# Performance work log

Hardware: AMD Instinct MI355X
Metric: run time of the kernel (lower is better)

## Reference

```python
import jax, jax.numpy as jnp
import numpy as np

B, N, HID, EPOCH = 16, 512, 32, 201


def setup_inputs() -> dict:
    key = jax.random.key(0)
    k1, k2, k3, k4 = jax.random.split(key, 4)
    f = jax.random.normal(k1, (B, 1, N, N), dtype=jnp.float32)
    # per-sample 3x3 stencil: perturbed 5-point Laplacian, positive center for stable Jacobi
    base = jnp.array([[0., -1., 0.], [-1., 4., -1.], [0., -1., 0.]], dtype=jnp.float32)
    kernelA = base[None, None] + 0.1 * jax.random.normal(k2, (B, 1, 3, 3), dtype=jnp.float32)
    kernelA = kernelA.at[:, :, 1, 1].set(jnp.maximum(kernelA[:, :, 1, 1], 1.0))
    u = jnp.zeros((B, 1, N, N), jnp.float32)
    # stand-in DeepONet H: pointwise 2 -> HID -> 1 MLP on concat(LFA, residual)
    W1 = 0.1 * jax.random.normal(k3, (HID, 2), dtype=jnp.float32)
    b1 = jnp.zeros((HID,), jnp.float32)
    W2 = 0.1 * jax.random.normal(k4, (1, HID), dtype=jnp.float32)
    b2 = jnp.zeros((1,), jnp.float32)
    return {"f": f, "kernelA": kernelA, "u": u, "W1": W1, "b1": b1, "W2": W2, "b2": b2, "epoch": EPOCH}


def _A(x, kernel):
    # per-sample 3x3 stencil: batch dim mapped to channels, grouped conv (groups = B)
    bsz = x.shape[0]
    y = jax.lax.conv_general_dilated(
        jnp.transpose(x, (1, 0, 2, 3)), kernel, (1, 1), ((1, 1), (1, 1)),
        dimension_numbers=("NCHW", "OIHW", "NCHW"), feature_group_count=bsz)
    return jnp.transpose(y, (1, 0, 2, 3))


def _lfa(kernelA, n):
    # ComputeSmootherFactor: Jacobi symbol |prod_j (1 - tau * A_hat(theta))| on the frequency grid
    h = 1.0 / (n + 1)
    p = np.arange(-(n // 2), n // 2)
    P1, P2 = np.meshgrid(p, p)
    t1 = jnp.asarray(2j * np.pi * h * P1, jnp.complex64)
    t2 = jnp.asarray(2j * np.pi * h * P2, jnp.complex64)
    E = jnp.stack([
        jnp.exp(-t1 - t2), jnp.exp(-t2), jnp.exp(t1 - t2),
        jnp.exp(-t1), jnp.ones_like(t1), jnp.exp(t1),
        jnp.exp(-t1 + t2), jnp.exp(t2), jnp.exp(t1 + t2)])  # [9,N,N]
    bsz = kernelA.shape[0]
    S = jnp.einsum("bk,kxy->bxy", kernelA.reshape(bsz, 9).astype(jnp.complex64), E)
    tau = (0.5 / kernelA[:, 0, 1, 1]).astype(jnp.complex64)[:, None, None]
    y = (1.0 - tau * S) ** 5  # 5 identical Jacobi factors
    return jnp.abs(y)[:, None].astype(jnp.float32)  # [B,1,N,N]


def _H(lfa, r, W1, b1, W2, b2):
    # pointwise MLP correction operator (stand-in for DeepONet)
    z = jnp.concatenate([lfa, r], axis=1)  # [B,2,N,N]
    hdn = jax.nn.gelu(jnp.einsum("bcxy,oc->boxy", z, W1) + b1[None, :, None, None])
    return jnp.einsum("bcxy,oc->boxy", hdn, W2) + b2[None, :, None, None]


def reference(f, kernelA, u, W1, b1, W2, b2, epoch):
    K = (epoch - 1) // 100 + 1
    n = f.shape[-1]
    lfa = _lfa(kernelA, n)
    taus = 0.5 / kernelA[:, :, 1:2, 1:2]  # [B,1,1,1], w=0.5
    x = jnp.zeros_like(f)
    for _ in range(K):
        for _ in range(10):  # jacobi, M=10
            x = x + taus * (f - _A(x, kernelA))
        r = f - _A(x, kernelA)
        x = x + _H(lfa, r, W1, b1, W2, b2)
    r = f - _A(x, kernelA)
    return jnp.linalg.norm(r) / jnp.linalg.norm(f)
```

## Files before the change

### kernel.cpp

```cpp
#include <hip/hip_runtime.h>
#include <math.h>

#define BB 16
#define NN 512
#define HID 32

#define HALO 16
#define TW 96
#define TWP 97
#define OT 64

#define GELU_K1 (-2.302208201f)
#define GELU_K2 (-0.102944244f)

#define CDR 0.99992499f
#define SDR 0.012247618f
#define REVS 0.0019493177f

__global__ __launch_bounds__(256) void lfa_kernel(const float* __restrict__ kernelA,
                                                  float* __restrict__ lfa) {
    const int t = threadIdx.x;
    const int strip = t & 127;
    const int i = blockIdx.y * 2 + (t >> 7);
    const int b = blockIdx.z;
    const int j0 = strip * 4;
    const float* a = kernelA + b * 9;
    float a0 = a[0], a1 = a[1], a2 = a[2], a3 = a[3], a4 = a[4];
    float a5 = a[5], a6 = a[6], a7 = a[7], a8 = a[8];
    const float A35 = a3 + a5, A17 = a1 + a7, A08 = a0 + a8, A26 = a2 + a6;
    const float B53 = a5 - a3, B71 = a7 - a1, B80 = a8 - a0, B26 = a2 - a6;
    const float tau = 0.5f / a4;

    float r1 = (float)(j0 - NN / 2) * REVS;
    float r2 = (float)(i - NN / 2) * REVS;
    float s1 = __builtin_amdgcn_sinf(r1);
    float c1 = __builtin_amdgcn_cosf(r1);
    float s2 = __builtin_amdgcn_sinf(r2);
    float c2 = __builtin_amdgcn_cosf(r2);

    float out[4];
#pragma unroll
    for (int k = 0; k < 4; ++k) {
        float cc = c1 * c2, ss = s1 * s2, sc = s1 * c2, cs = c1 * s2;
        float cpp = cc - ss, cpm = cc + ss, spp = sc + cs, spm = sc - cs;
        float re = fmaf(A35, c1, a4); re = fmaf(A17, c2, re);
        re = fmaf(A08, cpp, re);      re = fmaf(A26, cpm, re);
        float im = B53 * s1;          im = fmaf(B71, s2, im);
        im = fmaf(B80, spp, im);      im = fmaf(B26, spm, im);
        float zre = fmaf(-tau, re, 1.0f);
        float zim = tau * im;
        float m2 = fmaf(zre, zre, zim * zim);
        out[k] = m2 * m2 * sqrtf(m2);
        float tt = s1 * SDR;
        float ns = fmaf(s1, CDR, c1 * SDR);
        c1 = fmaf(c1, CDR, -tt);
        s1 = ns;
    }
    float4 ov = {out[0], out[1], out[2], out[3]};
    *(float4*)(lfa + (size_t)b * NN * NN + (size_t)i * NN + j0) = ov;
}

template <bool FIRST, bool RES>
__global__ __launch_bounds__(256) void fused_cycle(
        const float* __restrict__ xin, float* __restrict__ xout,
        const float* __restrict__ f, const float* __restrict__ kernelA,
        const float* __restrict__ lfa,
        const float* __restrict__ W1, const float* __restrict__ b1,
        const float* __restrict__ W2, const float* __restrict__ b2,
        float* __restrict__ accp, float* __restrict__ outp) {
    __shared__ float sxraw[98 * TWP + 2];
    float* sx = sxraw + TWP + 1;
    const int tx = threadIdx.x;
    const int ty = threadIdx.y;
    const int t  = ty * 32 + tx;
    const int b  = blockIdx.z;
    const int gy0 = blockIdx.y * OT;
    const int gx0 = blockIdx.x * OT;
    const int goi = gy0 - HALO;
    const int goj = gx0 - HALO;
    const float* fg = f + (size_t)b * NN * NN;
    const float* ag = kernelA + b * 9;
    const float ar0 = ag[0], ar1 = ag[1], ar2 = ag[2], ar3 = ag[3], ar4 = ag[4];
    const float ar5 = ag[5], ar6 = ag[6], ar7 = ag[7], ar8 = ag[8];
    const float tau = 0.5f / ar4;
    const float s0 = tau * ar0, q1 = tau * ar1, q2 = tau * ar2, q3 = tau * ar3;
    const float q4 = tau * ar4, q5 = tau * ar5, q6 = tau * ar6, q7 = tau * ar7;
    const float q8 = tau * ar8;

    if (FIRST) {
        if (t == 0 && (blockIdx.x | blockIdx.y | blockIdx.z) == 0) {
            accp[0] = 0.f;
            accp[1] = 0.f;
            ((unsigned int*)accp)[2] = 0u;
        }
    }

    if (t < 98) sxraw[t] = 0.f;
    if (t < 96) sxraw[97 + 97 * t] = 0.f;
    if (t < 98) sxraw[9409 + t] = 0.f;

    if (!FIRST) {
        const float* xg = xin + (size_t)b * NN * NN;
#pragma unroll
        for (int k = 0; k < 9; ++k) {
            int idx = t + k * 256;
            int row = idx / 24;
            int c4  = (idx - row * 24) * 4;
            int gi = goi + row, gj = goj + c4;
            float4 v = {0.f, 0.f, 0.f, 0.f};
            if ((unsigned)gi < NN && (unsigned)gj < NN)
                v = *(const float4*)(xg + (size_t)gi * NN + gj);
            float* d = sx + row * TWP + c4;
            d[0] = v.x; d[1] = v.y; d[2] = v.z; d[3] = v.w;
        }
    }

    const int R0 = ty * 12, C0 = tx * 3;

    const float* pb  = sx + (R0 - 1) * TWP + (C0 - 1);
    float*       pwv = sx + R0 * TWP + C0;

    float vR[12], vC[3];
#pragma unroll
    for (int r = 0; r < 12; ++r) {
        int R = R0 + r, gi = goi + R;
        vR[r] = (R >= 1 && R < TW - 1 && gi >= 0 && gi < NN) ? 1.f : 0.f;
    }
#pragma unroll
    for (int c = 0; c < 3; ++c) {
        int C = C0 + c, gj = goj + C;
        vC[c] = (C >= 1 && C < TW - 1 && gj >= 0 && gj < NN) ? 1.f : 0.f;
    }

    float frt[12][3];
#pragma unroll
    for (int r = 0; r < 12; ++r) {
        int gi = goi + R0 + r;
#pragma unroll
        for (int c = 0; c < 3; ++c) {
            int gj = goj + C0 + c;
            frt[r][c] = (gi >= 0 && gi < NN && gj >= 0 && gj < NN)
                            ? tau * fg[gi * NN + gj] : 0.f;
        }
    }

    __syncthreads();

    float cur[12][3];
    if (FIRST) {
#pragma unroll
        for (int r = 0; r < 12; ++r) {
#pragma unroll
            for (int c = 0; c < 3; ++c)
                cur[r][c] = (vR[r] * vC[c]) * frt[r][c];
        }
        pwv[0] = cur[0][0]; pwv[1] = cur[0][1]; pwv[2] = cur[0][2];
        pwv[11 * TWP] = cur[11][0]; pwv[11 * TWP + 1] = cur[11][1];
        pwv[11 * TWP + 2] = cur[11][2];
#pragma unroll
        for (int r = 1; r < 11; ++r) {
            pwv[r * TWP] = cur[r][0];
            pwv[r * TWP + 2] = cur[r][2];
        }
        __syncthreads();
    } else {
#pragma unroll
        for (int r = 0; r < 12; ++r) {
            cur[r][0] = pwv[r * TWP];
            cur[r][1] = pwv[r * TWP + 1];
            cur[r][2] = pwv[r * TWP + 2];
        }
    }

    for (int s = FIRST ? 1 : 0; s < 10; ++s) {
        float top0 = pb[0], top1 = pb[1], top2 = pb[2], top3 = pb[3], top4 = pb[4];
        float bot0 = pb[13 * TWP],     bot1 = pb[13 * TWP + 1],
              bot2 = pb[13 * TWP + 2], bot3 = pb[13 * TWP + 3],
              bot4 = pb[13 * TWP + 4];
        float pm0 = top1, pm1v = top2, pm2 = top3;
        float Lm1 = top0, Rm1 = top4;
        float Lc = pb[TWP], Rc = pb[TWP + 4];
#pragma unroll
        for (int r = 0; r < 12; ++r) {
            float n0, n1, n2, Lp, Rp;
            if (r < 11) {
                n0 = cur[r + 1][0]; n1 = cur[r + 1][1]; n2 = cur[r + 1][2];
                Lp = pb[(r + 2) * TWP];
                Rp = pb[(r + 2) * TWP + 4];
            } else {
                n0 = bot1; n1 = bot2; n2 = bot3; Lp = bot0; Rp = bot4;
            }
            float o0 = cur[r][0], o1 = cur[r][1], o2 = cur[r][2];
            {
                float ax = s0 * Lm1;
                ax = fmaf(q1, pm0, ax); ax = fmaf(q2, pm1v, ax);
                ax = fmaf(q3, Lc, ax);  ax = fmaf(q4, o0, ax);
                ax = fmaf(q5, o1, ax);  ax = fmaf(q6, Lp, ax);
                ax = fmaf(q7, n0, ax);  ax = fmaf(q8, n1, ax);
                cur[r][0] = fmaf(vR[r] * vC[0], frt[r][0] - ax, o0);
            }
            {
                float ax = s0 * pm0;
                ax = fmaf(q1, pm1v, ax); ax = fmaf(q2, pm2, ax);
                ax = fmaf(q3, o0, ax);   ax = fmaf(q4, o1, ax);
                ax = fmaf(q5, o2, ax);   ax = fmaf(q6, n0, ax);
                ax = fmaf(q7, n1, ax);   ax = fmaf(q8, n2, ax);
                cur[r][1] = fmaf(vR[r] * vC[1], frt[r][1] - ax, o1);
            }
            {
                float ax = s0 * pm1v;
                ax = fmaf(q1, pm2, ax); ax = fmaf(q2, Rm1, ax);
                ax = fmaf(q3, o1, ax);  ax = fmaf(q4, o2, ax);
                ax = fmaf(q5, Rc, ax);  ax = fmaf(q6, n1, ax);
                ax = fmaf(q8, Rp, fmaf(q7, n2, ax));
                cur[r][2] = fmaf(vR[r] * vC[2], frt[r][2] - ax, o2);
            }
            pm0 = o0; pm1v = o1; pm2 = o2;
            Lm1 = Lc; Rm1 = Rc; Lc = Lp; Rc = Rp;
        }
        __syncthreads();
        if (s < 9) {
            pwv[0] = cur[0][0]; pwv[1] = cur[0][1]; pwv[2] = cur[0][2];
            pwv[11 * TWP] = cur[11][0]; pwv[11 * TWP + 1] = cur[11][1];
            pwv[11 * TWP + 2] = cur[11][2];
#pragma unroll
            for (int r = 1; r < 11; ++r) {
                pwv[r * TWP] = cur[r][0];
                pwv[r * TWP + 2] = cur[r][2];
            }
        } else {
#pragma unroll
            for (int r = 0; r < 12; ++r) {
                pwv[r * TWP] = cur[r][0];
                pwv[r * TWP + 1] = cur[r][1];
                pwv[r * TWP + 2] = cur[r][2];
            }
        }
        __syncthreads();
    }

    const int orow = t >> 2;
    const int oseg = t & 3;
    const int Rl = HALO + orow;
    const int Cl0 = HALO + oseg * 16;
    const float* pw = sx + (Rl - 1) * TWP + (Cl0 - 1);
    const int gi = gy0 + orow;
    const int gjb = gx0 + oseg * 16;
    const float b2v = b2[0];

    if (!RES) {
        float w0[18], w1[18], w2[18];
#pragma unroll
        for (int k = 0; k < 18; ++k) {
            w0[k] = pw[k];
            w1[k] = pw[TWP + k];
            w2[k] = pw[2 * TWP + k];
        }
        const float4* f4 = (const float4*)(fg + (size_t)gi * NN + gjb);
        const float4* l4 = (const float4*)(lfa + (size_t)b * NN * NN + (size_t)gi * NN + gjb);
        float fv[16], lv[16];
#pragma unroll
        for (int q = 0; q < 4; ++q) {
            float4 fq = f4[q], lq = l4[q];
            fv[q * 4] = fq.x; fv[q * 4 + 1] = fq.y; fv[q * 4 + 2] = fq.z; fv[q * 4 + 3] = fq.w;
            lv[q * 4] = lq.x; lv[q * 4 + 1] = lq.y; lv[q * 4 + 2] = lq.z; lv[q * 4 + 3] = lq.w;
        }
        float rv[16];
#pragma unroll
        for (int k = 0; k < 16; ++k) {
            float ax = ar0 * w0[k];
            ax = fmaf(ar1, w0[k + 1], ax); ax = fmaf(ar2, w0[k + 2], ax);
            ax = fmaf(ar3, w1[k], ax);     ax = fmaf(ar4, w1[k + 1], ax);
            ax = fmaf(ar5, w1[k + 2], ax); ax = fmaf(ar6, w2[k], ax);
            ax = fmaf(ar7, w2[k + 1], ax); ax = fmaf(ar8, w2[k + 2], ax);
            rv[k] = fv[k] - ax;
        }
        float acc[16];
#pragma unroll
        for (int k = 0; k < 16; ++k) acc[k] = 0.f;
        for (int hh = 0; hh < HID; ++hh) {
            float w1a = W1[2 * hh], w1b = W1[2 * hh + 1], bb = b1[hh], wo = W2[hh];
#pragma unroll
            for (int k = 0; k < 16; ++k) {
                float v = fmaf(w1a, lv[k], fmaf(w1b, rv[k], bb));
                float m = v * fmaf(GELU_K2, v * v, GELU_K1);
                float e = __builtin_amdgcn_exp2f(m);
                float g = v * __builtin_amdgcn_rcpf(1.0f + e);
                acc[k] = fmaf(wo, g, acc[k]);
            }
        }
        float4* xo4 = (float4*)(xout + (size_t)b * NN * NN + (size_t)gi * NN + gjb);
#pragma unroll
        for (int q = 0; q < 4; ++q) {
            float4 ov;
            ov.x = w1[q * 4 + 1] + acc[q * 4] + b2v;
            ov.y = w1[q * 4 + 2] + acc[q * 4 + 1] + b2v;
            ov.z = w1[q * 4 + 3] + acc[q * 4 + 2] + b2v;
            ov.w = w1[q * 4 + 4] + acc[q * 4 + 3] + b2v;
            xo4[q] = ov;
        }
    } else {
        float rv[16];
        {
            float w[18];
#pragma unroll
            for (int k = 0; k < 18; ++k) w[k] = pw[k];
#pragma unroll
            for (int k = 0; k < 16; ++k) {
                float ax = ar0 * w[k];
                ax = fmaf(ar1, w[k + 1], ax);
                rv[k] = fmaf(ar2, w[k + 2], ax);
            }
#pragma unroll
            for (int k = 0; k < 18; ++k) w[k] = pw[TWP + k];
#pragma unroll
            for (int k = 0; k < 16; ++k) {
                float ax = fmaf(ar3, w[k], rv[k]);
                ax = fmaf(ar4, w[k + 1], ax);
                rv[k] = fmaf(ar5, w[k + 2], ax);
            }
#pragma unroll
            for (int k = 0; k < 18; ++k) w[k] = pw[2 * TWP + k];
#pragma unroll
            for (int k = 0; k < 16; ++k) {
                float ax = fmaf(ar6, w[k], rv[k]);
                ax = fmaf(ar7, w[k + 1], ax);
                rv[k] = fmaf(ar8, w[k + 2], ax);
            }
        }
        float f2 = 0.f;
        {
            const float4* f4 = (const float4*)(fg + (size_t)gi * NN + gjb);
#pragma unroll
            for (int q = 0; q < 4; ++q) {
                float4 fq = f4[q];
                rv[q * 4]     = fq.x - rv[q * 4];
                rv[q * 4 + 1] = fq.y - rv[q * 4 + 1];
                rv[q * 4 + 2] = fq.z - rv[q * 4 + 2];
                rv[q * 4 + 3] = fq.w - rv[q * 4 + 3];
                f2 = fmaf(fq.x, fq.x, f2);
                f2 = fmaf(fq.y, fq.y, f2);
                f2 = fmaf(fq.z, fq.z, f2);
                f2 = fmaf(fq.w, fq.w, f2);
            }
        }

        float Hr0 = 0.f, Hr1 = 0.f;
        int hoff0 = 0, hoff1 = 0;
        auto ringH = [&](int rc, float& Hv, int& hoff) {
            int R, C;
            if (rc < 66)       { R = 15; C = 15 + rc; }
            else if (rc < 132) { R = 80; C = rc - 51; }
            else if (rc < 196) { R = rc - 116; C = 15; }
            else               { R = rc - 180; C = 80; }
            hoff = R * TWP + C;
            int rgi = goi + R, rgj = goj + C;
            Hv = 0.f;
            if (rgi >= 0 && rgi < NN && rgj >= 0 && rgj < NN) {
                const float* pr = sx + (R - 1) * TWP + (C - 1);
                float u0 = pr[0], u1 = pr[1], u2 = pr[2];
                float m0 = pr[TWP], m1 = pr[TWP + 1], m2 = pr[TWP + 2];
                float d0 = pr[2 * TWP], d1 = pr[2 * TWP + 1], d2 = pr[2 * TWP + 2];
                float ax = ar0 * u0;
                ax = fmaf(ar1, u1, ax); ax = fmaf(ar2, u2, ax);
                ax = fmaf(ar3, m0, ax); ax = fmaf(ar4, m1, ax);
                ax = fmaf(ar5, m2, ax); ax = fmaf(ar6, d0, ax);
                ax = fmaf(ar7, d1, ax); ax = fmaf(ar8, d2, ax);
                float rp = fg[(size_t)rgi * NN + rgj] - ax;
                float lf = lfa[(size_t)b * NN * NN + (size_t)rgi * NN + rgj];
                float av = 0.f;
                for (int hh = 0; hh < HID; ++hh) {
                    float w1a = W1[2 * hh], w1b = W1[2 * hh + 1], bbv = b1[hh], wo = W2[hh];
                    float v = fmaf(w1a, lf, fmaf(w1b, rp, bbv));
                    float m = v * fmaf(GELU_K2, v * v, GELU_K1);
                    float e = __builtin_amdgcn_exp2f(m);
                    float gg = v * __builtin_amdgcn_rcpf(1.0f + e);
                    av = fmaf(wo, gg, av);
                }
                Hv = av + b2v;
            }
        };
        ringH(t, Hr0, hoff0);
        if (t < 4) ringH(t + 256, Hr1, hoff1);

        float acc[16];
#pragma unroll
        for (int k = 0; k < 16; ++k) acc[k] = 0.f;
        {
            float lv[16];
            const float4* l4 = (const float4*)(lfa + (size_t)b * NN * NN + (size_t)gi * NN + gjb);
#pragma unroll
            for (int q = 0; q < 4; ++q) {
                float4 lq = l4[q];
                lv[q * 4] = lq.x; lv[q * 4 + 1] = lq.y;
                lv[q * 4 + 2] = lq.z; lv[q * 4 + 3] = lq.w;
            }
            for (int hh = 0; hh < HID; ++hh) {
                float w1a = W1[2 * hh], w1b = W1[2 * hh + 1], bb = b1[hh], wo = W2[hh];
#pragma unroll
                for (int k = 0; k < 16; ++k) {
                    float v = fmaf(w1a, lv[k], fmaf(w1b, rv[k], bb));
                    float m = v * fmaf(GELU_K2, v * v, GELU_K1);
                    float e = __builtin_amdgcn_exp2f(m);
                    float g = v * __builtin_amdgcn_rcpf(1.0f + e);
                    acc[k] = fmaf(wo, g, acc[k]);
                }
            }
        }

        __syncthreads();
        float* ph = sx + Rl * TWP + Cl0;
#pragma unroll
        for (int k = 0; k < 16; ++k) ph[k] = acc[k] + b2v;
        sx[hoff0] = Hr0;
        if (t < 4) sx[hoff1] = Hr1;
        __syncthreads();

        float rr = 0.f;
        {
            float hr[18];
#pragma unroll
            for (int k = 0; k < 18; ++k) hr[k] = pw[k];
#pragma unroll
            for (int k = 0; k < 16; ++k) {
                float ax = ar0 * hr[k];
                ax = fmaf(ar1, hr[k + 1], ax);
                ax = fmaf(ar2, hr[k + 2], ax);
                rv[k] -= ax;
            }
#pragma unroll
            for (int k = 0; k < 18; ++k) hr[k] = pw[TWP + k];
#pragma unroll
            for (int k = 0; k < 16; ++k) {
                float ax = ar3 * hr[k];
                ax = fmaf(ar4, hr[k + 1], ax);
                ax = fmaf(ar5, hr[k + 2], ax);
                rv[k] -= ax;
            }
#pragma unroll
            for (int k = 0; k < 18; ++k) hr[k] = pw[2 * TWP + k];
#pragma unroll
            for (int k = 0; k < 16; ++k) {
                float ax = ar6 * hr[k];
                ax = fmaf(ar7, hr[k + 1], ax);
                ax = fmaf(ar8, hr[k + 2], ax);
                float r = rv[k] - ax;
                rr = fmaf(r, r, rr);
            }
        }
#pragma unroll
        for (int off = 32; off > 0; off >>= 1) {
            rr += __shfl_down(rr, off, 64);
            f2 += __shfl_down(f2, off, 64);
        }
        if ((t & 63) == 0) { sxraw[t >> 6] = rr; sxraw[4 + (t >> 6)] = f2; }
        __syncthreads();
        if (t == 0) {
            atomicAdd(&accp[0], sxraw[0] + sxraw[1] + sxraw[2] + sxraw[3]);
            atomicAdd(&accp[1], sxraw[4] + sxraw[5] + sxraw[6] + sxraw[7]);
            __threadfence();
            unsigned int done = atomicAdd((unsigned int*)accp + 2, 1u);
            if (done == (NN / OT) * (NN / OT) * BB - 1) {
                __threadfence();
                float rrt = atomicAdd(&accp[0], 0.f);
                float fft = atomicAdd(&accp[1], 0.f);
                outp[0] = sqrtf(rrt / fft);
            }
        }
    }
}

extern "C" void kernel_launch(void* const* d_in, const int* in_sizes, int n_in,
                              void* d_out, int out_size, void* d_ws, size_t ws_size,
                              hipStream_t stream) {
    const float* f  = (const float*)d_in[0];
    const float* kA = (const float*)d_in[1];
    float*       u  = (float*)d_in[2];
    const float* W1 = (const float*)d_in[3];
    const float* b1 = (const float*)d_in[4];
    const float* W2 = (const float*)d_in[5];
    const float* b2 = (const float*)d_in[6];
    float* out = (float*)d_out;

    char* ws = (char*)d_ws;
    float* acc = (float*)ws;
    float* xB  = (float*)(ws + 256);
    float* lfa = (float*)(ws + 256 + (size_t)BB * NN * NN * 4);

    lfa_kernel<<<dim3(1, NN / 2, BB), 256, 0, stream>>>(kA, lfa);

    dim3 jblk(32, 8);
    dim3 jgrd(NN / OT, NN / OT, BB);

    fused_cycle<true,  false><<<jgrd, jblk, 0, stream>>>(u, xB, f, kA, lfa, W1, b1, W2, b2, acc, out);
    fused_cycle<false, false><<<jgrd, jblk, 0, stream>>>(xB, u, f, kA, lfa, W1, b1, W2, b2, acc, out);
    fused_cycle<false, true ><<<jgrd, jblk, 0, stream>>>(u, xB, f, kA, lfa, W1, b1, W2, b2, acc, out);
}
```

Baseline: 362.2 us.

## Exchange column halos via wave shuffles and double-buffer row halos in LDS

Within the fused Jacobi sweep, left and right neighbour columns now come from cross-lane shuffles instead of shared-memory reads. Only the top and bottom boundary rows of each thread's 12-row strip are published, into a separate ping-pong LDS region. Alternating buffers leaves one barrier per sweep instead of two, and the shared-memory writeback is reduced to the final sweep. The risk is at wave edges: a lane at the edge of a 64-lane wave gets a wrong or zero neighbour unless the halo masking covers it, and the shuffles add cross-lane instruction cost.

```diff
diff --git a/kernel.cpp b/kernel.cpp
--- a/kernel.cpp
+++ b/kernel.cpp
@@ -16,6 +16,9 @@
 #define CDR 0.99992499f
 #define SDR 0.012247618f
 #define REVS 0.0019493177f
+
+#define PUBA 194
+#define PUBDP 2328
 
 __global__ __launch_bounds__(256) void lfa_kernel(const float* __restrict__ kernelA,
                                                   float* __restrict__ lfa) {
@@ -95,11 +98,28 @@
         }
     }
 
-    if (t < 98) sxraw[t] = 0.f;
-    if (t < 96) sxraw[97 + 97 * t] = 0.f;
-    if (t < 98) sxraw[9409 + t] = 0.f;
+    auto pub_zero = [&]() {
+        for (int idx = t; idx < 448; idx += 256) {
+            int p = (idx >= 224) ? 1 : 0;
+            int j = idx - (p ? 224 : 0);
+            int off;
+            if (j < 98) off = PUBA + j;
+            else if (j < 196) off = 2044 + (j - 98);
+            else {
+                int g = j - 196;
+                int s, base;
+                if (g < 14) { base = PUBA; s = 1 + (g >> 1); }
+                else        { base = 1358; s = (g - 14) >> 1; }
+                off = base + s * 98 + ((g & 1) ? 97 : 0);
+            }
+            sxraw[off + (p ? PUBDP : 0)] = 0.f;
+        }
+    };
 
     if (!FIRST) {
+        if (t < 98) sxraw[t] = 0.f;
+        if (t < 96) sxraw[97 + 97 * t] = 0.f;
+        if (t < 98) sxraw[9409 + t] = 0.f;
         const float* xg = xin + (size_t)b * NN * NN;
 #pragma unroll
         for (int k = 0; k < 9; ++k) {
@@ -113,12 +133,14 @@
             float* d = sx + row * TWP + c4;
             d[0] = v.x; d[1] = v.y; d[2] = v.z; d[3] = v.w;
         }
+    } else {
+        pub_zero();
     }
 
     const int R0 = ty * 12, C0 = tx * 3;
-
     const float* pb  = sx + (R0 - 1) * TWP + (C0 - 1);
     float*       pwv = sx + R0 * TWP + C0;
+    float*       PT  = sxraw + PUBA + ty * 98 + C0;
 
     float vR[12], vC[3];
 #pragma unroll
@@ -144,49 +166,21 @@
         }
     }
 
-    __syncthreads();
-
     float cur[12][3];
-    if (FIRST) {
-#pragma unroll
-        for (int r = 0; r < 12; ++r) {
-#pragma unroll
-            for (int c = 0; c < 3; ++c)
-                cur[r][c] = (vR[r] * vC[c]) * frt[r][c];
-        }
-        pwv[0] = cur[0][0]; pwv[1] = cur[0][1]; pwv[2] = cur[0][2];
-        pwv[11 * TWP] = cur[11][0]; pwv[11 * TWP + 1] = cur[11][1];
-        pwv[11 * TWP + 2] = cur[11][2];
-#pragma unroll
-        for (int r = 1; r < 11; ++r) {
-            pwv[r * TWP] = cur[r][0];
-            pwv[r * TWP + 2] = cur[r][2];
-        }
-        __syncthreads();
-    } else {
-#pragma unroll
-        for (int r = 0; r < 12; ++r) {
-            cur[r][0] = pwv[r * TWP];
-            cur[r][1] = pwv[r * TWP + 1];
-            cur[r][2] = pwv[r * TWP + 2];
-        }
-    }
-
-    for (int s = FIRST ? 1 : 0; s < 10; ++s) {
-        float top0 = pb[0], top1 = pb[1], top2 = pb[2], top3 = pb[3], top4 = pb[4];
-        float bot0 = pb[13 * TWP],     bot1 = pb[13 * TWP + 1],
-              bot2 = pb[13 * TWP + 2], bot3 = pb[13 * TWP + 3],
-              bot4 = pb[13 * TWP + 4];
+
+    auto sweep_core = [&](float top0, float top1, float top2, float top3, float top4,
+                          float bot0, float bot1, float bot2, float bot3, float bot4) {
         float pm0 = top1, pm1v = top2, pm2 = top3;
         float Lm1 = top0, Rm1 = top4;
-        float Lc = pb[TWP], Rc = pb[TWP + 4];
+        float Lc = __shfl_up(cur[0][2], 1);
+        float Rc = __shfl_down(cur[0][0], 1);
 #pragma unroll
         for (int r = 0; r < 12; ++r) {
             float n0, n1, n2, Lp, Rp;
             if (r < 11) {
                 n0 = cur[r + 1][0]; n1 = cur[r + 1][1]; n2 = cur[r + 1][2];
-                Lp = pb[(r + 2) * TWP];
-                Rp = pb[(r + 2) * TWP + 4];
+                Lp = __shfl_up(cur[r + 1][2], 1);
+                Rp = __shfl_down(cur[r + 1][0], 1);
             } else {
                 n0 = bot1; n1 = bot2; n2 = bot3; Lp = bot0; Rp = bot4;
             }
@@ -212,32 +206,61 @@
                 ax = fmaf(q1, pm2, ax); ax = fmaf(q2, Rm1, ax);
                 ax = fmaf(q3, o1, ax);  ax = fmaf(q4, o2, ax);
                 ax = fmaf(q5, Rc, ax);  ax = fmaf(q6, n1, ax);
-                ax = fmaf(q8, Rp, fmaf(q7, n2, ax));
+                ax = fmaf(q7, n2, ax);  ax = fmaf(q8, Rp, ax);
                 cur[r][2] = fmaf(vR[r] * vC[2], frt[r][2] - ax, o2);
             }
             pm0 = o0; pm1v = o1; pm2 = o2;
             Lm1 = Lc; Rm1 = Rc; Lc = Lp; Rc = Rp;
         }
+    };
+
+    auto pub_rows = [&](float* wB) {
+        if (ty < 7) { wB[0] = cur[11][0]; wB[1] = cur[11][1]; wB[2] = cur[11][2]; }
+        if (ty > 0) { wB[968] = cur[0][0]; wB[969] = cur[0][1]; wB[970] = cur[0][2]; }
+    };
+
+    if (FIRST) {
+#pragma unroll
+        for (int r = 0; r < 12; ++r)
+#pragma unroll
+            for (int c = 0; c < 3; ++c)
+                cur[r][c] = (vR[r] * vC[c]) * frt[r][c];
+    } else {
         __syncthreads();
-        if (s < 9) {
-            pwv[0] = cur[0][0]; pwv[1] = cur[0][1]; pwv[2] = cur[0][2];
-            pwv[11 * TWP] = cur[11][0]; pwv[11 * TWP + 1] = cur[11][1];
-            pwv[11 * TWP + 2] = cur[11][2];
-#pragma unroll
-            for (int r = 1; r < 11; ++r) {
-                pwv[r * TWP] = cur[r][0];
-                pwv[r * TWP + 2] = cur[r][2];
-            }
-        } else {
-#pragma unroll
-            for (int r = 0; r < 12; ++r) {
-                pwv[r * TWP] = cur[r][0];
-                pwv[r * TWP + 1] = cur[r][1];
-                pwv[r * TWP + 2] = cur[r][2];
-            }
+#pragma unroll
+        for (int r = 0; r < 12; ++r) {
+            cur[r][0] = pwv[r * TWP];
+            cur[r][1] = pwv[r * TWP + 1];
+            cur[r][2] = pwv[r * TWP + 2];
         }
         __syncthreads();
-    }
+        pub_zero();
+        sweep_core(pb[0], pb[1], pb[2], pb[3], pb[4],
+                   pb[13 * TWP], pb[13 * TWP + 1], pb[13 * TWP + 2],
+                   pb[13 * TWP + 3], pb[13 * TWP + 4]);
+    }
+    pub_rows(PT + 99);
+    __syncthreads();
+
+    int e = PUBDP;
+    for (int s = 1; s < 9; ++s) {
+        sweep_core(PT[0], PT[1], PT[2], PT[3], PT[4],
+                   PT[1164], PT[1165], PT[1166], PT[1167], PT[1168]);
+        pub_rows(PT + 99 + e);
+        PT += e; e = -e;
+        __syncthreads();
+    }
+
+    sweep_core(PT[0], PT[1], PT[2], PT[3], PT[4],
+               PT[1164], PT[1165], PT[1166], PT[1167], PT[1168]);
+    __syncthreads();
+#pragma unroll
+    for (int r = 0; r < 12; ++r) {
+        pwv[r * TWP] = cur[r][0];
+        pwv[r * TWP + 1] = cur[r][1];
+        pwv[r * TWP + 2] = cur[r][2];
+    }
+    __syncthreads();
 
     const int orow = t >> 2;
     const int oseg = t & 3;
@@ -284,8 +307,8 @@
             for (int k = 0; k < 16; ++k) {
                 float v = fmaf(w1a, lv[k], fmaf(w1b, rv[k], bb));
                 float m = v * fmaf(GELU_K2, v * v, GELU_K1);
-                float e = __builtin_amdgcn_exp2f(m);
-                float g = v * __builtin_amdgcn_rcpf(1.0f + e);
+                float e2 = __builtin_amdgcn_exp2f(m);
+                float g = v * __builtin_amdgcn_rcpf(1.0f + e2);
                 acc[k] = fmaf(wo, g, acc[k]);
             }
         }
@@ -373,8 +396,8 @@
                     float w1a = W1[2 * hh], w1b = W1[2 * hh + 1], bbv = b1[hh], wo = W2[hh];
                     float v = fmaf(w1a, lf, fmaf(w1b, rp, bbv));
                     float m = v * fmaf(GELU_K2, v * v, GELU_K1);
-                    float e = __builtin_amdgcn_exp2f(m);
-                    float gg = v * __builtin_amdgcn_rcpf(1.0f + e);
+                    float e2 = __builtin_amdgcn_exp2f(m);
+                    float gg = v * __builtin_amdgcn_rcpf(1.0f + e2);
                     av = fmaf(wo, gg, av);
                 }
                 Hv = av + b2v;
@@ -401,8 +424,8 @@
                 for (int k = 0; k < 16; ++k) {
                     float v = fmaf(w1a, lv[k], fmaf(w1b, rv[k], bb));
                     float m = v * fmaf(GELU_K2, v * v, GELU_K1);
-                    float e = __builtin_amdgcn_exp2f(m);
-                    float g = v * __builtin_amdgcn_rcpf(1.0f + e);
+                    float e2 = __builtin_amdgcn_exp2f(m);
+                    float g = v * __builtin_amdgcn_rcpf(1.0f + e2);
                     acc[k] = fmaf(wo, g, acc[k]);
                 }
             }
```

Result: no change. 366.3 us (+1.1%).

## Double threads per block, halve rows per thread, use shuffles for horizontal halos

Applied to the files above, without the earlier changes.

The fused Jacobi/MLP kernel moves from 256 to 512 threads per block. Each thread now owns a 6x3 strip instead of 12x3, and the epilogue handles 8 columns per thread instead of 16. Left and right neighbour values inside the strip now come from wavefront shuffles instead of shared memory, so only the top and bottom rows of each strip are written back to LDS between sweeps. The aim is fewer registers per thread, more active waves and less LDS traffic, at the cost of more barrier participants and shuffle instructions.

```diff
diff --git a/kernel.cpp b/kernel.cpp
--- a/kernel.cpp
+++ b/kernel.cpp
@@ -61,7 +61,7 @@
 }
 
 template <bool FIRST, bool RES>
-__global__ __launch_bounds__(256) void fused_cycle(
+__global__ __launch_bounds__(512) void fused_cycle(
         const float* __restrict__ xin, float* __restrict__ xout,
         const float* __restrict__ f, const float* __restrict__ kernelA,
         const float* __restrict__ lfa,
@@ -102,27 +102,28 @@
     if (!FIRST) {
         const float* xg = xin + (size_t)b * NN * NN;
 #pragma unroll
-        for (int k = 0; k < 9; ++k) {
-            int idx = t + k * 256;
-            int row = idx / 24;
-            int c4  = (idx - row * 24) * 4;
-            int gi = goi + row, gj = goj + c4;
-            float4 v = {0.f, 0.f, 0.f, 0.f};
-            if ((unsigned)gi < NN && (unsigned)gj < NN)
-                v = *(const float4*)(xg + (size_t)gi * NN + gj);
-            float* d = sx + row * TWP + c4;
-            d[0] = v.x; d[1] = v.y; d[2] = v.z; d[3] = v.w;
-        }
-    }
-
-    const int R0 = ty * 12, C0 = tx * 3;
-
+        for (int k = 0; k < 5; ++k) {
+            int idx = t + k * 512;
+            if (idx < 2304) {
+                int row = idx / 24;
+                int c4  = (idx - row * 24) * 4;
+                int gi = goi + row, gj = goj + c4;
+                float4 v = {0.f, 0.f, 0.f, 0.f};
+                if ((unsigned)gi < NN && (unsigned)gj < NN)
+                    v = *(const float4*)(xg + (size_t)gi * NN + gj);
+                float* d = sx + row * TWP + c4;
+                d[0] = v.x; d[1] = v.y; d[2] = v.z; d[3] = v.w;
+            }
+        }
+    }
+
+    const int R0 = ty * 6, C0 = tx * 3;
     const float* pb  = sx + (R0 - 1) * TWP + (C0 - 1);
     float*       pwv = sx + R0 * TWP + C0;
 
-    float vR[12], vC[3];
-#pragma unroll
-    for (int r = 0; r < 12; ++r) {
+    float vR[6], vC[3];
+#pragma unroll
+    for (int r = 0; r < 6; ++r) {
         int R = R0 + r, gi = goi + R;
         vR[r] = (R >= 1 && R < TW - 1 && gi >= 0 && gi < NN) ? 1.f : 0.f;
     }
@@ -132,9 +133,9 @@
         vC[c] = (C >= 1 && C < TW - 1 && gj >= 0 && gj < NN) ? 1.f : 0.f;
     }
 
-    float frt[12][3];
-#pragma unroll
-    for (int r = 0; r < 12; ++r) {
+    float frt[6][3];
+#pragma unroll
+    for (int r = 0; r < 6; ++r) {
         int gi = goi + R0 + r;
 #pragma unroll
         for (int c = 0; c < 3; ++c) {
@@ -146,26 +147,20 @@
 
     __syncthreads();
 
-    float cur[12][3];
+    float cur[6][3];
     if (FIRST) {
 #pragma unroll
-        for (int r = 0; r < 12; ++r) {
+        for (int r = 0; r < 6; ++r)
 #pragma unroll
             for (int c = 0; c < 3; ++c)
                 cur[r][c] = (vR[r] * vC[c]) * frt[r][c];
-        }
         pwv[0] = cur[0][0]; pwv[1] = cur[0][1]; pwv[2] = cur[0][2];
-        pwv[11 * TWP] = cur[11][0]; pwv[11 * TWP + 1] = cur[11][1];
-        pwv[11 * TWP + 2] = cur[11][2];
-#pragma unroll
-        for (int r = 1; r < 11; ++r) {
-            pwv[r * TWP] = cur[r][0];
-            pwv[r * TWP + 2] = cur[r][2];
-        }
+        pwv[5 * TWP] = cur[5][0]; pwv[5 * TWP + 1] = cur[5][1];
+        pwv[5 * TWP + 2] = cur[5][2];
         __syncthreads();
     } else {
 #pragma unroll
-        for (int r = 0; r < 12; ++r) {
+        for (int r = 0; r < 6; ++r) {
             cur[r][0] = pwv[r * TWP];
             cur[r][1] = pwv[r * TWP + 1];
             cur[r][2] = pwv[r * TWP + 2];
@@ -174,19 +169,20 @@
 
     for (int s = FIRST ? 1 : 0; s < 10; ++s) {
         float top0 = pb[0], top1 = pb[1], top2 = pb[2], top3 = pb[3], top4 = pb[4];
-        float bot0 = pb[13 * TWP],     bot1 = pb[13 * TWP + 1],
-              bot2 = pb[13 * TWP + 2], bot3 = pb[13 * TWP + 3],
-              bot4 = pb[13 * TWP + 4];
+        float bot0 = pb[7 * TWP],     bot1 = pb[7 * TWP + 1],
+              bot2 = pb[7 * TWP + 2], bot3 = pb[7 * TWP + 3],
+              bot4 = pb[7 * TWP + 4];
         float pm0 = top1, pm1v = top2, pm2 = top3;
         float Lm1 = top0, Rm1 = top4;
-        float Lc = pb[TWP], Rc = pb[TWP + 4];
-#pragma unroll
-        for (int r = 0; r < 12; ++r) {
+        float Lc = __shfl_up(cur[0][2], 1);
+        float Rc = __shfl_down(cur[0][0], 1);
+#pragma unroll
+        for (int r = 0; r < 6; ++r) {
             float n0, n1, n2, Lp, Rp;
-            if (r < 11) {
+            if (r < 5) {
                 n0 = cur[r + 1][0]; n1 = cur[r + 1][1]; n2 = cur[r + 1][2];
-                Lp = pb[(r + 2) * TWP];
-                Rp = pb[(r + 2) * TWP + 4];
+                Lp = __shfl_up(cur[r + 1][2], 1);
+                Rp = __shfl_down(cur[r + 1][0], 1);
             } else {
                 n0 = bot1; n1 = bot2; n2 = bot3; Lp = bot0; Rp = bot4;
             }
@@ -212,7 +208,7 @@
                 ax = fmaf(q1, pm2, ax); ax = fmaf(q2, Rm1, ax);
                 ax = fmaf(q3, o1, ax);  ax = fmaf(q4, o2, ax);
                 ax = fmaf(q5, Rc, ax);  ax = fmaf(q6, n1, ax);
-                ax = fmaf(q8, Rp, fmaf(q7, n2, ax));
+                ax = fmaf(q7, n2, ax);  ax = fmaf(q8, Rp, ax);
                 cur[r][2] = fmaf(vR[r] * vC[2], frt[r][2] - ax, o2);
             }
             pm0 = o0; pm1v = o1; pm2 = o2;
@@ -221,16 +217,11 @@
         __syncthreads();
         if (s < 9) {
             pwv[0] = cur[0][0]; pwv[1] = cur[0][1]; pwv[2] = cur[0][2];
-            pwv[11 * TWP] = cur[11][0]; pwv[11 * TWP + 1] = cur[11][1];
-            pwv[11 * TWP + 2] = cur[11][2];
-#pragma unroll
-            for (int r = 1; r < 11; ++r) {
-                pwv[r * TWP] = cur[r][0];
-                pwv[r * TWP + 2] = cur[r][2];
-            }
+            pwv[5 * TWP] = cur[5][0]; pwv[5 * TWP + 1] = cur[5][1];
+            pwv[5 * TWP + 2] = cur[5][2];
         } else {
 #pragma unroll
-            for (int r = 0; r < 12; ++r) {
+            for (int r = 0; r < 6; ++r) {
                 pwv[r * TWP] = cur[r][0];
                 pwv[r * TWP + 1] = cur[r][1];
                 pwv[r * TWP + 2] = cur[r][2];
@@ -239,35 +230,35 @@
         __syncthreads();
     }
 
-    const int orow = t >> 2;
-    const int oseg = t & 3;
+    const int orow = t >> 3;
+    const int oseg = t & 7;
     const int Rl = HALO + orow;
-    const int Cl0 = HALO + oseg * 16;
+    const int Cl0 = HALO + oseg * 8;
     const float* pw = sx + (Rl - 1) * TWP + (Cl0 - 1);
     const int gi = gy0 + orow;
-    const int gjb = gx0 + oseg * 16;
+    const int gjb = gx0 + oseg * 8;
     const float b2v = b2[0];
 
     if (!RES) {
-        float w0[18], w1[18], w2[18];
-#pragma unroll
-        for (int k = 0; k < 18; ++k) {
+        float w0[10], w1[10], w2[10];
+#pragma unroll
+        for (int k = 0; k < 10; ++k) {
             w0[k] = pw[k];
             w1[k] = pw[TWP + k];
             w2[k] = pw[2 * TWP + k];
         }
         const float4* f4 = (const float4*)(fg + (size_t)gi * NN + gjb);
         const float4* l4 = (const float4*)(lfa + (size_t)b * NN * NN + (size_t)gi * NN + gjb);
-        float fv[16], lv[16];
-#pragma unroll
-        for (int q = 0; q < 4; ++q) {
+        float fv[8], lv[8];
+#pragma unroll
+        for (int q = 0; q < 2; ++q) {
             float4 fq = f4[q], lq = l4[q];
             fv[q * 4] = fq.x; fv[q * 4 + 1] = fq.y; fv[q * 4 + 2] = fq.z; fv[q * 4 + 3] = fq.w;
             lv[q * 4] = lq.x; lv[q * 4 + 1] = lq.y; lv[q * 4 + 2] = lq.z; lv[q * 4 + 3] = lq.w;
         }
-        float rv[16];
-#pragma unroll
-        for (int k = 0; k < 16; ++k) {
+        float rv[8];
+#pragma unroll
+        for (int k = 0; k < 8; ++k) {
             float ax = ar0 * w0[k];
             ax = fmaf(ar1, w0[k + 1], ax); ax = fmaf(ar2, w0[k + 2], ax);
             ax = fmaf(ar3, w1[k], ax);     ax = fmaf(ar4, w1[k + 1], ax);
@@ -275,23 +266,23 @@
             ax = fmaf(ar7, w2[k + 1], ax); ax = fmaf(ar8, w2[k + 2], ax);
             rv[k] = fv[k] - ax;
         }
-        float acc[16];
-#pragma unroll
-        for (int k = 0; k < 16; ++k) acc[k] = 0.f;
+        float acc[8];
+#pragma unroll
+        for (int k = 0; k < 8; ++k) acc[k] = 0.f;
         for (int hh = 0; hh < HID; ++hh) {
             float w1a = W1[2 * hh], w1b = W1[2 * hh + 1], bb = b1[hh], wo = W2[hh];
 #pragma unroll
-            for (int k = 0; k < 16; ++k) {
+            for (int k = 0; k < 8; ++k) {
                 float v = fmaf(w1a, lv[k], fmaf(w1b, rv[k], bb));
                 float m = v * fmaf(GELU_K2, v * v, GELU_K1);
-                float e = __builtin_amdgcn_exp2f(m);
-                float g = v * __builtin_amdgcn_rcpf(1.0f + e);
+                float e2 = __builtin_amdgcn_exp2f(m);
+                float g = v * __builtin_amdgcn_rcpf(1.0f + e2);
                 acc[k] = fmaf(wo, g, acc[k]);
             }
         }
         float4* xo4 = (float4*)(xout + (size_t)b * NN * NN + (size_t)gi * NN + gjb);
 #pragma unroll
-        for (int q = 0; q < 4; ++q) {
+        for (int q = 0; q < 2; ++q) {
             float4 ov;
             ov.x = w1[q * 4 + 1] + acc[q * 4] + b2v;
             ov.y = w1[q * 4 + 2] + acc[q * 4 + 1] + b2v;
@@ -300,29 +291,29 @@
             xo4[q] = ov;
         }
     } else {
-        float rv[16];
+        float rv[8];
         {
-            float w[18];
-#pragma unroll
-            for (int k = 0; k < 18; ++k) w[k] = pw[k];
-#pragma unroll
-            for (int k = 0; k < 16; ++k) {
+            float w[10];
+#pragma unroll
+            for (int k = 0; k < 10; ++k) w[k] = pw[k];
+#pragma unroll
+            for (int k = 0; k < 8; ++k) {
                 float ax = ar0 * w[k];
                 ax = fmaf(ar1, w[k + 1], ax);
                 rv[k] = fmaf(ar2, w[k + 2], ax);
             }
 #pragma unroll
-            for (int k = 0; k < 18; ++k) w[k] = pw[TWP + k];
-#pragma unroll
-            for (int k = 0; k < 16; ++k) {
+            for (int k = 0; k < 10; ++k) w[k] = pw[TWP + k];
+#pragma unroll
+            for (int k = 0; k < 8; ++k) {
                 float ax = fmaf(ar3, w[k], rv[k]);
                 ax = fmaf(ar4, w[k + 1], ax);
                 rv[k] = fmaf(ar5, w[k + 2], ax);
             }
 #pragma unroll
-            for (int k = 0; k < 18; ++k) w[k] = pw[2 * TWP + k];
-#pragma unroll
-            for (int k = 0; k < 16; ++k) {
+            for (int k = 0; k < 10; ++k) w[k] = pw[2 * TWP + k];
+#pragma unroll
+            for (int k = 0; k < 8; ++k) {
                 float ax = fmaf(ar6, w[k], rv[k]);
                 ax = fmaf(ar7, w[k + 1], ax);
                 rv[k] = fmaf(ar8, w[k + 2], ax);
@@ -332,7 +323,7 @@
         {
             const float4* f4 = (const float4*)(fg + (size_t)gi * NN + gjb);
 #pragma unroll
-            for (int q = 0; q < 4; ++q) {
+            for (int q = 0; q < 2; ++q) {
                 float4 fq = f4[q];
                 rv[q * 4]     = fq.x - rv[q * 4];
                 rv[q * 4 + 1] = fq.y - rv[q * 4 + 1];
@@ -345,17 +336,16 @@
             }
         }
 
-        float Hr0 = 0.f, Hr1 = 0.f;
-        int hoff0 = 0, hoff1 = 0;
-        auto ringH = [&](int rc, float& Hv, int& hoff) {
+        float Hr0 = 0.f;
+        int hoff0 = 0;
+        if (t < 260) {
             int R, C;
-            if (rc < 66)       { R = 15; C = 15 + rc; }
-            else if (rc < 132) { R = 80; C = rc - 51; }
-            else if (rc < 196) { R = rc - 116; C = 15; }
-            else               { R = rc - 180; C = 80; }
-            hoff = R * TWP + C;
+            if (t < 66)        { R = 15; C = 15 + t; }
+            else if (t < 132)  { R = 80; C = t - 51; }
+            else if (t < 196)  { R = t - 116; C = 15; }
+            else               { R = t - 180; C = 80; }
+            hoff0 = R * TWP + C;
             int rgi = goi + R, rgj = goj + C;
-            Hv = 0.f;
             if (rgi >= 0 && rgi < NN && rgj >= 0 && rgj < NN) {
                 const float* pr = sx + (R - 1) * TWP + (C - 1);
                 float u0 = pr[0], u1 = pr[1], u2 = pr[2];
@@ -373,24 +363,22 @@
                     float w1a = W1[2 * hh], w1b = W1[2 * hh + 1], bbv = b1[hh], wo = W2[hh];
                     float v = fmaf(w1a, lf, fmaf(w1b, rp, bbv));
                     float m = v * fmaf(GELU_K2, v * v, GELU_K1);
-                    float e = __builtin_amdgcn_exp2f(m);
-                    float gg = v * __builtin_amdgcn_rcpf(1.0f + e);
+                    float e2 = __builtin_amdgcn_exp2f(m);
+                    float gg = v * __builtin_amdgcn_rcpf(1.0f + e2);
                     av = fmaf(wo, gg, av);
                 }
-                Hv = av + b2v;
-            }
-        };
-        ringH(t, Hr0, hoff0);
-        if (t < 4) ringH(t + 256, Hr1, hoff1);
-
-        float acc[16];
-#pragma unroll
-        for (int k = 0; k < 16; ++k) acc[k] = 0.f;
+                Hr0 = av + b2v;
+            }
+        }
+
+        float acc[8];
+#pragma unroll
+        for (int k = 0; k < 8; ++k) acc[k] = 0.f;
         {
-            float lv[16];
+            float lv[8];
             const float4* l4 = (const float4*)(lfa + (size_t)b * NN * NN + (size_t)gi * NN + gjb);
 #pragma unroll
-            for (int q = 0; q < 4; ++q) {
+            for (int q = 0; q < 2; ++q) {
                 float4 lq = l4[q];
                 lv[q * 4] = lq.x; lv[q * 4 + 1] = lq.y;
                 lv[q * 4 + 2] = lq.z; lv[q * 4 + 3] = lq.w;
@@ -398,11 +386,11 @@
             for (int hh = 0; hh < HID; ++hh) {
                 float w1a = W1[2 * hh], w1b = W1[2 * hh + 1], bb = b1[hh], wo = W2[hh];
 #pragma unroll
-                for (int k = 0; k < 16; ++k) {
+                for (int k = 0; k < 8; ++k) {
                     float v = fmaf(w1a, lv[k], fmaf(w1b, rv[k], bb));
                     float m = v * fmaf(GELU_K2, v * v, GELU_K1);
-                    float e = __builtin_amdgcn_exp2f(m);
-                    float g = v * __builtin_amdgcn_rcpf(1.0f + e);
+                    float e2 = __builtin_amdgcn_exp2f(m);
+                    float g = v * __builtin_amdgcn_rcpf(1.0f + e2);
                     acc[k] = fmaf(wo, g, acc[k]);
                 }
             }
@@ -411,36 +399,35 @@
         __syncthreads();
         float* ph = sx + Rl * TWP + Cl0;
 #pragma unroll
-        for (int k = 0; k < 16; ++k) ph[k] = acc[k] + b2v;
-        sx[hoff0] = Hr0;
-        if (t < 4) sx[hoff1] = Hr1;
+        for (int k = 0; k < 8; ++k) ph[k] = acc[k] + b2v;
+        if (t < 260) sx[hoff0] = Hr0;
         __syncthreads();
 
         float rr = 0.f;
         {
-            float hr[18];
-#pragma unroll
-            for (int k = 0; k < 18; ++k) hr[k] = pw[k];
-#pragma unroll
-            for (int k = 0; k < 16; ++k) {
+            float hr[10];
+#pragma unroll
+            for (int k = 0; k < 10; ++k) hr[k] = pw[k];
+#pragma unroll
+            for (int k = 0; k < 8; ++k) {
                 float ax = ar0 * hr[k];
                 ax = fmaf(ar1, hr[k + 1], ax);
                 ax = fmaf(ar2, hr[k + 2], ax);
                 rv[k] -= ax;
             }
 #pragma unroll
-            for (int k = 0; k < 18; ++k) hr[k] = pw[TWP + k];
-#pragma unroll
-            for (int k = 0; k < 16; ++k) {
+            for (int k = 0; k < 10; ++k) hr[k] = pw[TWP + k];
+#pragma unroll
+            for (int k = 0; k < 8; ++k) {
                 float ax = ar3 * hr[k];
                 ax = fmaf(ar4, hr[k + 1], ax);
                 ax = fmaf(ar5, hr[k + 2], ax);
                 rv[k] -= ax;
             }
 #pragma unroll
-            for (int k = 0; k < 18; ++k) hr[k] = pw[2 * TWP + k];
-#pragma unroll
-            for (int k = 0; k < 16; ++k) {
+            for (int k = 0; k < 10; ++k) hr[k] = pw[2 * TWP + k];
+#pragma unroll
+            for (int k = 0; k < 8; ++k) {
                 float ax = ar6 * hr[k];
                 ax = fmaf(ar7, hr[k + 1], ax);
                 ax = fmaf(ar8, hr[k + 2], ax);
@@ -453,11 +440,14 @@
             rr += __shfl_down(rr, off, 64);
             f2 += __shfl_down(f2, off, 64);
         }
-        if ((t & 63) == 0) { sxraw[t >> 6] = rr; sxraw[4 + (t >> 6)] = f2; }
+        if ((t & 63) == 0) { sxraw[t >> 6] = rr; sxraw[8 + (t >> 6)] = f2; }
         __syncthreads();
         if (t == 0) {
-            atomicAdd(&accp[0], sxraw[0] + sxraw[1] + sxraw[2] + sxraw[3]);
-            atomicAdd(&accp[1], sxraw[4] + sxraw[5] + sxraw[6] + sxraw[7]);
+            float sr = 0.f, sf = 0.f;
+#pragma unroll
+            for (int wv = 0; wv < 8; ++wv) { sr += sxraw[wv]; sf += sxraw[8 + wv]; }
+            atomicAdd(&accp[0], sr);
+            atomicAdd(&accp[1], sf);
             __threadfence();
             unsigned int done = atomicAdd((unsigned int*)accp + 2, 1u);
             if (done == (NN / OT) * (NN / OT) * BB - 1) {
@@ -489,7 +479,7 @@
 
     lfa_kernel<<<dim3(1, NN / 2, BB), 256, 0, stream>>>(kA, lfa);
 
-    dim3 jblk(32, 8);
+    dim3 jblk(32, 16);
     dim3 jgrd(NN / OT, NN / OT, BB);
 
     fused_cycle<true,  false><<<jgrd, jblk, 0, stream>>>(u, xB, f, kA, lfa, W1, b1, W2, b2, acc, out);
```

Result: slower. 382.7 us (+5.6%).
